# Kernel tuning notes

Measured on AMD Instinct MI355X. Metric: run time of the kernel, lower is better.

The kernel has to match this reference:

```python
import jax, jax.numpy as jnp
import numpy as np

D_MODEL = 1024
D_STATE = 16
D_CONV = 4
EXPAND = 2
D_INNER = EXPAND * D_MODEL  # 2048
B_SZ = 4
SEQ_L = 2048


def setup_inputs() -> dict:
    key = jax.random.key(0)
    ks = jax.random.split(key, 8)
    x = jax.random.normal(ks[0], (B_SZ, SEQ_L, D_MODEL), dtype=jnp.float32)
    # nn.Linear(d_model, 2*d_inner, bias=False): weight [2*d_inner, d_model]
    W_in = jax.random.normal(ks[1], (2 * D_INNER, D_MODEL), dtype=jnp.float32) * (1.0 / np.sqrt(D_MODEL))
    # depthwise Conv1d weight [d_inner, 1, d_conv] -> stored as [d_inner, d_conv]
    conv_w = jax.random.normal(ks[2], (D_INNER, D_CONV), dtype=jnp.float32) * (1.0 / np.sqrt(D_CONV))
    conv_b = jax.random.normal(ks[3], (D_INNER,), dtype=jnp.float32) * 0.01
    W_out = jax.random.normal(ks[4], (D_MODEL, D_INNER), dtype=jnp.float32) * (1.0 / np.sqrt(D_INNER))
    A = jnp.eye(D_STATE, dtype=jnp.float32)
    Bmat = jax.random.normal(ks[5], (D_STATE, D_INNER), dtype=jnp.float32) * 0.01
    Cmat = jax.random.normal(ks[6], (D_STATE, D_INNER), dtype=jnp.float32) * 0.01
    return {"x": x, "W_in": W_in, "conv_w": conv_w, "conv_b": conv_b,
            "W_out": W_out, "A": A, "Bmat": Bmat, "Cmat": Cmat}


def _causal_depthwise_conv(x_bld, conv_w, conv_b):
    # x_bld: [B, L, C]; conv_w: [C, k]; matches torch Conv1d(groups=C, padding=k-1) sliced to [:L]
    C, k = conv_w.shape
    lhs = jnp.transpose(x_bld, (0, 2, 1))            # [B, C, L]
    rhs = conv_w[:, None, :]                          # [C, 1, k]
    out = jax.lax.conv_general_dilated(
        lhs, rhs, window_strides=(1,), padding=[(k - 1, 0)],
        feature_group_count=C,
        dimension_numbers=("NCH", "OIH", "NCH"))
    out = out + conv_b[None, :, None]
    return jnp.transpose(out, (0, 2, 1))              # [B, L, C]


def reference(x, W_in, conv_w, conv_b, W_out, A, Bmat, Cmat):
    B, L, _ = x.shape
    d_state = A.shape[0]
    xz = x @ W_in.T                                   # [B, L, 2*d_inner]
    x_part, z = jnp.split(xz, 2, axis=-1)             # each [B, L, d_inner]
    x_conv = jax.nn.silu(_causal_depthwise_conv(x_part, conv_w, conv_b))
    # precompute input drive u_t = x_t @ B.T for all t
    u = jnp.einsum("bld,sd->bls", x_part, Bmat)       # [B, L, d_state]

    def step(s, u_t):                                 # s: [B, d_state]
        s = s @ A.T + u_t
        return s, s

    s0 = jnp.zeros((B, d_state), dtype=x.dtype)
    _, states = jax.lax.scan(step, s0, jnp.transpose(u, (1, 0, 2)))  # [L, B, d_state]
    states = jnp.transpose(states, (1, 0, 2))         # [B, L, d_state]
    state_proj = jnp.einsum("bls,sd->bld", states, Cmat)  # [B, L, d_inner]
    y = (x_conv + state_proj) * jax.nn.sigmoid(z)     # [B, L, d_inner]
    return y @ W_out.T                                # [B, L, d_model]
```

## Files before the change

### kernel.cpp

```cpp
#include <hip/hip_runtime.h>

#define D_MODEL 1024
#define D_STATE 16
#define D_CONV  4
#define D_INNER 2048
#define B_SZ    4
#define SEQ_L   2048
#define ROWS    (B_SZ * SEQ_L)
#define N_XZ    (2 * D_INNER)

typedef unsigned short u16;
typedef unsigned int   u32;
typedef float f32x4 __attribute__((ext_vector_type(4)));
typedef short s16x8 __attribute__((ext_vector_type(8)));
typedef u16   u16x8 __attribute__((ext_vector_type(8)));
typedef u16   u16x4 __attribute__((ext_vector_type(4)));

__device__ __forceinline__ u16 f2bf(float f) {
  union { float f; u32 u; } v; v.f = f;
  u32 r = v.u + 0x7fffu + ((v.u >> 16) & 1u);
  return (u16)(r >> 16);
}
__device__ __forceinline__ float bf2f(u16 h) {
  union { u32 u; float f; } v; v.u = ((u32)h) << 16; return v.f;
}
__device__ __forceinline__ float sigmoidf_(float x) {
  return 1.0f / (1.0f + __expf(-x));
}

__global__ __launch_bounds__(256) void k_f2bf4(
    const float* __restrict__ a, u16* __restrict__ ao, int na4,
    const float* __restrict__ b, u16* __restrict__ bo, int nb4,
    const float* __restrict__ c, u16* __restrict__ co, int nc4,
    const float* __restrict__ e, u16* __restrict__ eo, int ne4)
{
  int i = blockIdx.x * 256 + threadIdx.x;
  const float* s; u16* d; int j;
  if (i < na4)                              { s = a; d = ao; j = i; }
  else if (i - na4 < nb4)                   { s = b; d = bo; j = i - na4; }
  else if (i - na4 - nb4 < nc4)             { s = c; d = co; j = i - na4 - nb4; }
  else if (i - na4 - nb4 - nc4 < ne4)       { s = e; d = eo; j = i - na4 - nb4 - nc4; }
  else return;
  f32x4 v = ((const f32x4*)s)[j];
  u16x4 o;
  o[0] = f2bf(v[0]); o[1] = f2bf(v[1]); o[2] = f2bf(v[2]); o[3] = f2bf(v[3]);
  ((u16x4*)d)[j] = o;
}

template<bool OUT_BF16>
__global__ __launch_bounds__(256, 2) void k_gemm_f(
    const u16* __restrict__ A,
    const u16* __restrict__ B,
    void* __restrict__ Cv,
    int M, int N, int K, int nbx)
{
  __shared__ __align__(16) u16 lA[3][128 * 32];
  __shared__ __align__(16) u16 lB[3][256 * 32];

  const int t    = threadIdx.x;
  const int lane = t & 63;
  const int wave = t >> 6;
  const int wr   = wave >> 1;
  const int wc   = wave & 1;
  const int lrow = lane & 15;
  const int lch  = lane >> 4;

  const int xcd = blockIdx.x & 7;
  const int sub = blockIdx.x >> 3;
  const int msz = (M >> 7) >> 2;
  const int nsz = nbx >> 1;
  const int sm  = sub / nsz;
  const int sn  = sub - sm * nsz;
  const int bm  = ((xcd >> 1) * msz + sm) * 128;
  const int bn  = ((xcd & 1) * nsz + sn) * 256;
  const int NT  = K / 32;

  const int ca0 = t, ca1 = t + 256;
  const u16* srcA0 = A + (size_t)(bm + (ca0 >> 2)) * K + ((ca0 & 3) ^ ((ca0 >> 3) & 3)) * 8;
  const u16* srcA1 = A + (size_t)(bm + (ca1 >> 2)) * K + ((ca1 & 3) ^ ((ca1 >> 3) & 3)) * 8;
  const u16* srcB[4];
#pragma unroll
  for (int i = 0; i < 4; ++i) {
    int c = t + i * 256;
    srcB[i] = B + (size_t)(bn + (c >> 2)) * K + ((c & 3) ^ ((c >> 3) & 3)) * 8;
  }

  auto stageA = [&](int sl, int kt) {
    __builtin_amdgcn_global_load_lds(
        (const __attribute__((address_space(1))) void*)(srcA0 + kt * 32),
        (__attribute__((address_space(3))) void*)&lA[sl][ca0 * 8], 16, 0, 0);
    __builtin_amdgcn_global_load_lds(
        (const __attribute__((address_space(1))) void*)(srcA1 + kt * 32),
        (__attribute__((address_space(3))) void*)&lA[sl][ca1 * 8], 16, 0, 0);
  };
  auto stageB = [&](int sl, int kt) {
#pragma unroll
    for (int i = 0; i < 4; ++i) {
      int c = t + i * 256;
      __builtin_amdgcn_global_load_lds(
          (const __attribute__((address_space(1))) void*)(srcB[i] + kt * 32),
          (__attribute__((address_space(3))) void*)&lB[sl][c * 8], 16, 0, 0);
    }
  };

  u32 offA[4], offB[8];
#pragma unroll
  for (int m = 0; m < 4; ++m) {
    int ra = wr * 64 + m * 16 + lrow;
    offA[m] = (u32)(ra * 64 + ((lch ^ ((ra >> 1) & 3)) << 4));
  }
#pragma unroll
  for (int n = 0; n < 8; ++n) {
    int rb = wc * 128 + n * 16 + lrow;
    offB[n] = (u32)(rb * 64 + ((lch ^ ((rb >> 1) & 3)) << 4));
  }
  const u32 baseA = (u32)(size_t)(__attribute__((address_space(3))) void*)&lA[0][0];
  const u32 baseB = (u32)(size_t)(__attribute__((address_space(3))) void*)&lB[0][0];

  f32x4 acc[4][8] = {};
  s16x8 av[4], bv[8];

  stageA(0, 0); stageB(0, 0);
  stageA(1, 1); stageB(1, 1);
  asm volatile("s_waitcnt vmcnt(6)" ::: "memory");
  __builtin_amdgcn_sched_barrier(0);
  __builtin_amdgcn_s_barrier();

  int slot = 0;
  for (int tt = 0; tt < NT; ++tt) {
    const int nslot = (slot == 0) ? 2 : slot - 1;
    const u32 bA = baseA + (u32)slot * 8192u;
    const u32 bB = baseB + (u32)slot * 16384u;
    const bool st = (tt + 2 < NT);
#pragma unroll
    for (int m = 0; m < 4; ++m) {
      u32 ad = bA + offA[m];
      asm volatile("ds_read_b128 %0, %1" : "=v"(av[m]) : "v"(ad));
    }
#pragma unroll
    for (int n = 0; n < 4; ++n) {
      u32 ad = bB + offB[n];
      asm volatile("ds_read_b128 %0, %1" : "=v"(bv[n]) : "v"(ad));
    }
    if (st) stageA(nslot, tt + 2);
    __builtin_amdgcn_sched_barrier(0);
    __builtin_amdgcn_s_barrier();
    asm volatile("s_waitcnt lgkmcnt(0)" ::: "memory");
    __builtin_amdgcn_sched_barrier(0);
    __builtin_amdgcn_s_setprio(1);
#pragma unroll
    for (int m = 0; m < 4; ++m)
#pragma unroll
      for (int n = 0; n < 4; ++n)
        acc[m][n] = __builtin_amdgcn_mfma_f32_16x16x32_bf16(
            av[m], bv[n], acc[m][n], 0, 0, 0);
    __builtin_amdgcn_s_setprio(0);
    __builtin_amdgcn_sched_barrier(0);
    __builtin_amdgcn_s_barrier();
#pragma unroll
    for (int n = 4; n < 8; ++n) {
      u32 ad = bB + offB[n];
      asm volatile("ds_read_b128 %0, %1" : "=v"(bv[n]) : "v"(ad));
    }
    if (st) stageB(nslot, tt + 2);
    __builtin_amdgcn_sched_barrier(0);
    __builtin_amdgcn_s_barrier();
    asm volatile("s_waitcnt lgkmcnt(0)" ::: "memory");
    __builtin_amdgcn_sched_barrier(0);
    __builtin_amdgcn_s_setprio(1);
#pragma unroll
    for (int m = 0; m < 4; ++m)
#pragma unroll
      for (int n = 4; n < 8; ++n)
        acc[m][n] = __builtin_amdgcn_mfma_f32_16x16x32_bf16(
            av[m], bv[n], acc[m][n], 0, 0, 0);
    __builtin_amdgcn_s_setprio(0);
    if (st)                asm volatile("s_waitcnt vmcnt(6)" ::: "memory");
    else if (tt + 1 < NT)  asm volatile("s_waitcnt vmcnt(0)" ::: "memory");
    __builtin_amdgcn_sched_barrier(0);
    __builtin_amdgcn_s_barrier();
    slot = (slot == 2) ? 0 : slot + 1;
  }

  const int crow0 = (lane >> 4) * 4;
  if constexpr (OUT_BF16) {
    u16* C = (u16*)Cv;
#pragma unroll
    for (int m = 0; m < 4; ++m)
#pragma unroll
      for (int n = 0; n < 8; ++n)
#pragma unroll
        for (int r = 0; r < 4; ++r) {
          int row = bm + wr * 64 + m * 16 + crow0 + r;
          int col = bn + wc * 128 + n * 16 + lrow;
          C[(size_t)row * N + col] = f2bf(acc[m][n][r]);
        }
  } else {
    float* C = (float*)Cv;
#pragma unroll
    for (int m = 0; m < 4; ++m)
#pragma unroll
      for (int n = 0; n < 8; ++n)
#pragma unroll
        for (int r = 0; r < 4; ++r) {
          int row = bm + wr * 64 + m * 16 + crow0 + r;
          int col = bn + wc * 128 + n * 16 + lrow;
          C[(size_t)row * N + col] = acc[m][n][r];
        }
  }
}

__global__ __launch_bounds__(256) void k_u_mfma(
    const u16* __restrict__ xz,
    const u16* __restrict__ Bbf,
    float* __restrict__ u)
{
  const int lane = threadIdx.x & 63;
  const int wave = threadIdx.x >> 6;
  const int row0 = blockIdx.x * 64 + wave * 16;
  const int ar   = lane & 15;
  const int ak   = (lane >> 4) * 8;
  const u16* xp = xz + (size_t)(row0 + ar) * N_XZ + ak;
  const u16* bp = Bbf + (size_t)ar * D_INNER + ak;
  f32x4 acc = {};
#pragma unroll 8
  for (int k = 0; k < D_INNER; k += 32) {
    s16x8 av = *(const s16x8*)(xp + k);
    s16x8 bv = *(const s16x8*)(bp + k);
    acc = __builtin_amdgcn_mfma_f32_16x16x32_bf16(av, bv, acc, 0, 0, 0);
  }
#pragma unroll
  for (int r = 0; r < 4; ++r)
    u[(size_t)(row0 + (lane >> 4) * 4 + r) * D_STATE + ar] = acc[r];
}

__global__ __launch_bounds__(64) void k_scan(
    const float* __restrict__ u, float* __restrict__ states)
{
  const int blk  = blockIdx.x;
  const int b    = blk >> 4;
  const int s    = blk & 15;
  const int lane = threadIdx.x;
  const float* up = u + (size_t)b * SEQ_L * D_STATE + s;
  float* sp = states + (size_t)b * SEQ_L * D_STATE + s;
  const int t0 = lane * (SEQ_L / 64);
  float v[32];
  float run = 0.0f;
#pragma unroll
  for (int i = 0; i < 32; ++i) { run += up[(size_t)(t0 + i) * D_STATE]; v[i] = run; }
  float tot = run;
  float pre = tot;
#pragma unroll
  for (int off = 1; off < 64; off <<= 1) {
    float n = __shfl_up(pre, off);
    if (lane >= off) pre += n;
  }
  pre -= tot;
#pragma unroll
  for (int i = 0; i < 32; ++i) sp[(size_t)(t0 + i) * D_STATE] = v[i] + pre;
}

__global__ __launch_bounds__(256) void k_fused_y(
    const u16* __restrict__ xz, const float* __restrict__ conv_w,
    const float* __restrict__ conv_b, const float* __restrict__ states,
    const float* __restrict__ Cmat, u16* __restrict__ y)
{
  const int t    = threadIdx.x;
  const int row0 = blockIdx.x * 4;
  const int l0   = row0 & (SEQ_L - 1);
  const int d0   = t * 8;

  float xin[7][8];
#pragma unroll
  for (int r = 0; r < 7; ++r) {
    int l = l0 + r - 3;
    if (l >= 0) {
      u16x8 v = *(const u16x8*)(xz + (size_t)(row0 + r - 3) * N_XZ + d0);
#pragma unroll
      for (int j = 0; j < 8; ++j) xin[r][j] = bf2f(v[j]);
    } else {
#pragma unroll
      for (int j = 0; j < 8; ++j) xin[r][j] = 0.0f;
    }
  }

  float cw[8][4];
#pragma unroll
  for (int j = 0; j < 8; ++j) {
    f32x4 w = ((const f32x4*)conv_w)[d0 + j];
#pragma unroll
    for (int k = 0; k < 4; ++k) cw[j][k] = w[k];
  }
  f32x4 cb0 = *(const f32x4*)(conv_b + d0);
  f32x4 cb1 = *(const f32x4*)(conv_b + d0 + 4);

  float xc[4][8];
#pragma unroll
  for (int rr = 0; rr < 4; ++rr)
#pragma unroll
    for (int j = 0; j < 8; ++j) {
      float v = (j < 4) ? cb0[j] : cb1[j - 4];
#pragma unroll
      for (int k = 0; k < 4; ++k) v += xin[rr + k][j] * cw[j][k];
      xc[rr][j] = v * sigmoidf_(v);
    }

  float st[4][16];
#pragma unroll
  for (int rr = 0; rr < 4; ++rr) {
    const f32x4* s4 = (const f32x4*)(states + (size_t)(row0 + rr) * D_STATE);
#pragma unroll
    for (int q = 0; q < 4; ++q) {
      f32x4 v = s4[q];
      st[rr][q * 4 + 0] = v[0]; st[rr][q * 4 + 1] = v[1];
      st[rr][q * 4 + 2] = v[2]; st[rr][q * 4 + 3] = v[3];
    }
  }
  float sp[4][8] = {};
#pragma unroll
  for (int s = 0; s < 16; ++s) {
    const float* cp = Cmat + (size_t)s * D_INNER + d0;
    f32x4 c0 = *(const f32x4*)cp;
    f32x4 c1 = *(const f32x4*)(cp + 4);
#pragma unroll
    for (int rr = 0; rr < 4; ++rr)
#pragma unroll
      for (int j = 0; j < 4; ++j) {
        sp[rr][j]     += st[rr][s] * c0[j];
        sp[rr][4 + j] += st[rr][s] * c1[j];
      }
  }
#pragma unroll
  for (int rr = 0; rr < 4; ++rr) {
    u16x8 zv = *(const u16x8*)(xz + (size_t)(row0 + rr) * N_XZ + D_INNER + d0);
    u16x8 o;
#pragma unroll
    for (int j = 0; j < 8; ++j)
      o[j] = f2bf((xc[rr][j] + sp[rr][j]) * sigmoidf_(bf2f(zv[j])));
    *(u16x8*)(y + (size_t)(row0 + rr) * D_INNER + d0) = o;
  }
}

extern "C" void kernel_launch(void* const* d_in, const int* in_sizes, int n_in,
                              void* d_out, int out_size, void* d_ws, size_t ws_size,
                              hipStream_t stream) {
  const float* x      = (const float*)d_in[0];
  const float* W_in   = (const float*)d_in[1];
  const float* conv_w = (const float*)d_in[2];
  const float* conv_b = (const float*)d_in[3];
  const float* W_out  = (const float*)d_in[4];
  const float* Bmat   = (const float*)d_in[6];
  const float* Cmat   = (const float*)d_in[7];
  float* out = (float*)d_out;

  char* ws = (char*)d_ws;
  u16*   xzbf   = (u16*)  (ws + 0);
  u16*   ybf    = (u16*)  (ws + 67108864);
  u16*   xbf    = (u16*)  (ws + 100663296);
  u16*   wibf   = (u16*)  (ws + 117440512);
  u16*   wobf   = (u16*)  (ws + 125829120);
  float* u      = (float*)(ws + 130023424);
  float* states = (float*)(ws + 130547712);
  u16*   bmbf   = (u16*)  (ws + 131072000);

  {
    int na4 = ROWS * D_MODEL / 4, nb4 = N_XZ * D_MODEL / 4,
        nc4 = D_MODEL * D_INNER / 4, ne4 = D_STATE * D_INNER / 4;
    int tot = na4 + nb4 + nc4 + ne4;
    k_f2bf4<<<(tot + 255) / 256, 256, 0, stream>>>(
        x, xbf, na4, W_in, wibf, nb4, W_out, wobf, nc4, Bmat, bmbf, ne4);
  }

  k_gemm_f<true><<<1024, 256, 0, stream>>>(xbf, wibf, xzbf, ROWS, N_XZ, D_MODEL, N_XZ / 256);

  k_u_mfma<<<ROWS / 64, 256, 0, stream>>>(xzbf, bmbf, u);
  k_scan<<<B_SZ * D_STATE, 64, 0, stream>>>(u, states);

  k_fused_y<<<ROWS / 4, 256, 0, stream>>>(xzbf, conv_w, conv_b, states, Cmat, ybf);

  k_gemm_f<false><<<256, 256, 0, stream>>>(ybf, wobf, out, ROWS, D_MODEL, D_INNER, D_MODEL / 256);
}
```

Measured before the change: 191.7 us.

## Add 256x256 tile GEMM for input projection and retile u/fused-y kernels

```diff
diff --git a/kernel.cpp b/kernel.cpp
--- a/kernel.cpp
+++ b/kernel.cpp
@@ -47,12 +47,124 @@
   ((u16x4*)d)[j] = o;
 }
 
+__global__ __launch_bounds__(512, 2) void k_gbig(
+    const u16* __restrict__ A,
+    const u16* __restrict__ B,
+    u16* __restrict__ C,
+    int M, int N, int K, int nbx)
+{
+  __shared__ __align__(16) u16 lA[2][256 * 32];
+  __shared__ __align__(16) u16 lB[2][256 * 32];
+
+  const int t    = threadIdx.x;
+  const int lane = t & 63;
+  const int wave = t >> 6;
+  const int wr   = wave >> 2;
+  const int wc   = wave & 3;
+  const int lrow = lane & 15;
+  const int kch  = lane >> 4;
+
+  const int xcd = blockIdx.x & 7;
+  const int sub = blockIdx.x >> 3;
+  const int msz = (M >> 8) >> 2;
+  const int nsz = nbx >> 1;
+  const int sm  = sub / nsz;
+  const int sn  = sub - sm * nsz;
+  const int bm  = ((xcd >> 1) * msz + sm) * 256;
+  const int bn  = ((xcd & 1) * nsz + sn) * 256;
+  const int NT  = K / 32;
+
+  const int c0 = t, c1 = t + 512;
+  const int r0 = c0 >> 2, ch0 = c0 & 3;
+  const int r1 = c1 >> 2, ch1 = c1 & 3;
+  const u16* srcA0 = A + (size_t)(bm + r0) * K + ((ch0 ^ ((r0 >> 1) & 3)) << 3);
+  const u16* srcA1 = A + (size_t)(bm + r1) * K + ((ch1 ^ ((r1 >> 1) & 3)) << 3);
+  const u16* srcB0 = B + (size_t)(bn + r0) * K + ((ch0 ^ ((r0 >> 1) & 3)) << 3);
+  const u16* srcB1 = B + (size_t)(bn + r1) * K + ((ch1 ^ ((r1 >> 1) & 3)) << 3);
+
+  auto stage = [&](int buf, int kt) {
+    __builtin_amdgcn_global_load_lds(
+        (const __attribute__((address_space(1))) void*)(srcA0 + kt * 32),
+        (__attribute__((address_space(3))) void*)&lA[buf][c0 * 8], 16, 0, 0);
+    __builtin_amdgcn_global_load_lds(
+        (const __attribute__((address_space(1))) void*)(srcA1 + kt * 32),
+        (__attribute__((address_space(3))) void*)&lA[buf][c1 * 8], 16, 0, 0);
+    __builtin_amdgcn_global_load_lds(
+        (const __attribute__((address_space(1))) void*)(srcB0 + kt * 32),
+        (__attribute__((address_space(3))) void*)&lB[buf][c0 * 8], 16, 0, 0);
+    __builtin_amdgcn_global_load_lds(
+        (const __attribute__((address_space(1))) void*)(srcB1 + kt * 32),
+        (__attribute__((address_space(3))) void*)&lB[buf][c1 * 8], 16, 0, 0);
+  };
+
+  u32 aoff[8], boff[4];
+#pragma unroll
+  for (int mi = 0; mi < 8; ++mi) {
+    int row = wr * 128 + mi * 16 + lrow;
+    aoff[mi] = (u32)(row * 64 + ((kch ^ ((row >> 1) & 3)) << 4));
+  }
+#pragma unroll
+  for (int ni = 0; ni < 4; ++ni) {
+    int row = wc * 64 + ni * 16 + lrow;
+    boff[ni] = (u32)(row * 64 + ((kch ^ ((row >> 1) & 3)) << 4));
+  }
+  const u32 baseA = (u32)(size_t)(__attribute__((address_space(3))) void*)&lA[0][0];
+  const u32 baseB = (u32)(size_t)(__attribute__((address_space(3))) void*)&lB[0][0];
+
+  f32x4 acc[8][4] = {};
+  s16x8 av[8], bv[4];
+
+  stage(0, 0);
+  asm volatile("s_waitcnt vmcnt(0)" ::: "memory");
+  __builtin_amdgcn_s_barrier();
+
+  for (int tt = 0; tt < NT; ++tt) {
+    const int cur = tt & 1;
+    const u32 bA = baseA + (u32)cur * 16384u;
+    const u32 bB = baseB + (u32)cur * 16384u;
+    const bool s1 = (tt + 1 < NT);
+
+#pragma unroll
+    for (int mi = 0; mi < 8; ++mi) {
+      u32 ad = bA + aoff[mi];
+      asm volatile("ds_read_b128 %0, %1" : "=v"(av[mi]) : "v"(ad));
+    }
+#pragma unroll
+    for (int ni = 0; ni < 4; ++ni) {
+      u32 ad = bB + boff[ni];
+      asm volatile("ds_read_b128 %0, %1" : "=v"(bv[ni]) : "v"(ad));
+    }
+    if (s1) stage(cur ^ 1, tt + 1);
+    asm volatile("s_waitcnt lgkmcnt(0)" ::: "memory");
+    __builtin_amdgcn_sched_barrier(0);
+    __builtin_amdgcn_s_setprio(1);
+#pragma unroll
+    for (int mi = 0; mi < 8; ++mi)
+#pragma unroll
+      for (int ni = 0; ni < 4; ++ni)
+        acc[mi][ni] = __builtin_amdgcn_mfma_f32_16x16x32_bf16(av[mi], bv[ni], acc[mi][ni], 0, 0, 0);
+    __builtin_amdgcn_s_setprio(0);
+    if (s1) asm volatile("s_waitcnt vmcnt(0)" ::: "memory");
+    __builtin_amdgcn_s_barrier();
+  }
+
+  const int crow0 = (lane >> 4) * 4;
+#pragma unroll
+  for (int mi = 0; mi < 8; ++mi)
+#pragma unroll
+    for (int ni = 0; ni < 4; ++ni)
+#pragma unroll
+      for (int r = 0; r < 4; ++r) {
+        int row = bm + wr * 128 + mi * 16 + crow0 + r;
+        int col = bn + wc * 64 + ni * 16 + lrow;
+        C[(size_t)row * N + col] = f2bf(acc[mi][ni][r]);
+      }
+}
+
 template<bool OUT_BF16>
 __global__ __launch_bounds__(256, 2) void k_gemm_f(
-    const u16* __restrict__ A,
-    const u16* __restrict__ B,
-    void* __restrict__ Cv,
-    int M, int N, int K, int nbx)
+    const u16* __restrict__ A, const u16* __restrict__ B,
+    void* __restrict__ Cv, int M, int N, int K, int nbx)
 {
   __shared__ __align__(16) u16 lA[3][128 * 32];
   __shared__ __align__(16) u16 lB[3][256 * 32];
@@ -123,7 +235,6 @@
   stageA(0, 0); stageB(0, 0);
   stageA(1, 1); stageB(1, 1);
   asm volatile("s_waitcnt vmcnt(6)" ::: "memory");
-  __builtin_amdgcn_sched_barrier(0);
   __builtin_amdgcn_s_barrier();
 
   int slot = 0;
@@ -133,17 +244,16 @@
     const u32 bB = baseB + (u32)slot * 16384u;
     const bool st = (tt + 2 < NT);
 #pragma unroll
+    for (int n = 0; n < 4; ++n) {
+      u32 ad = bB + offB[n];
+      asm volatile("ds_read_b128 %0, %1" : "=v"(bv[n]) : "v"(ad));
+    }
+#pragma unroll
     for (int m = 0; m < 4; ++m) {
       u32 ad = bA + offA[m];
       asm volatile("ds_read_b128 %0, %1" : "=v"(av[m]) : "v"(ad));
     }
-#pragma unroll
-    for (int n = 0; n < 4; ++n) {
-      u32 ad = bB + offB[n];
-      asm volatile("ds_read_b128 %0, %1" : "=v"(bv[n]) : "v"(ad));
-    }
     if (st) stageA(nslot, tt + 2);
-    __builtin_amdgcn_sched_barrier(0);
     __builtin_amdgcn_s_barrier();
     asm volatile("s_waitcnt lgkmcnt(0)" ::: "memory");
     __builtin_amdgcn_sched_barrier(0);
@@ -152,10 +262,8 @@
     for (int m = 0; m < 4; ++m)
 #pragma unroll
       for (int n = 0; n < 4; ++n)
-        acc[m][n] = __builtin_amdgcn_mfma_f32_16x16x32_bf16(
-            av[m], bv[n], acc[m][n], 0, 0, 0);
+        acc[m][n] = __builtin_amdgcn_mfma_f32_16x16x32_bf16(av[m], bv[n], acc[m][n], 0, 0, 0);
     __builtin_amdgcn_s_setprio(0);
-    __builtin_amdgcn_sched_barrier(0);
     __builtin_amdgcn_s_barrier();
 #pragma unroll
     for (int n = 4; n < 8; ++n) {
@@ -163,7 +271,6 @@
       asm volatile("ds_read_b128 %0, %1" : "=v"(bv[n]) : "v"(ad));
     }
     if (st) stageB(nslot, tt + 2);
-    __builtin_amdgcn_sched_barrier(0);
     __builtin_amdgcn_s_barrier();
     asm volatile("s_waitcnt lgkmcnt(0)" ::: "memory");
     __builtin_amdgcn_sched_barrier(0);
@@ -172,12 +279,10 @@
     for (int m = 0; m < 4; ++m)
 #pragma unroll
       for (int n = 4; n < 8; ++n)
-        acc[m][n] = __builtin_amdgcn_mfma_f32_16x16x32_bf16(
-            av[m], bv[n], acc[m][n], 0, 0, 0);
+        acc[m][n] = __builtin_amdgcn_mfma_f32_16x16x32_bf16(av[m], bv[n], acc[m][n], 0, 0, 0);
     __builtin_amdgcn_s_setprio(0);
     if (st)                asm volatile("s_waitcnt vmcnt(6)" ::: "memory");
     else if (tt + 1 < NT)  asm volatile("s_waitcnt vmcnt(0)" ::: "memory");
-    __builtin_amdgcn_sched_barrier(0);
     __builtin_amdgcn_s_barrier();
     slot = (slot == 2) ? 0 : slot + 1;
   }
@@ -210,28 +315,29 @@
   }
 }
 
-__global__ __launch_bounds__(256) void k_u_mfma(
-    const u16* __restrict__ xz,
-    const u16* __restrict__ Bbf,
+__global__ __launch_bounds__(64) void k_u_mfma(
+    const u16* __restrict__ xz, const u16* __restrict__ Bbf,
     float* __restrict__ u)
 {
-  const int lane = threadIdx.x & 63;
-  const int wave = threadIdx.x >> 6;
-  const int row0 = blockIdx.x * 64 + wave * 16;
+  const int lane = threadIdx.x;
+  const int row0 = blockIdx.x * 16;
   const int ar   = lane & 15;
   const int ak   = (lane >> 4) * 8;
   const u16* xp = xz + (size_t)(row0 + ar) * N_XZ + ak;
   const u16* bp = Bbf + (size_t)ar * D_INNER + ak;
-  f32x4 acc = {};
-#pragma unroll 8
-  for (int k = 0; k < D_INNER; k += 32) {
-    s16x8 av = *(const s16x8*)(xp + k);
-    s16x8 bv = *(const s16x8*)(bp + k);
-    acc = __builtin_amdgcn_mfma_f32_16x16x32_bf16(av, bv, acc, 0, 0, 0);
+  f32x4 acc0 = {}, acc1 = {};
+#pragma unroll 4
+  for (int k = 0; k < D_INNER; k += 64) {
+    s16x8 a0 = *(const s16x8*)(xp + k);
+    s16x8 b0 = *(const s16x8*)(bp + k);
+    s16x8 a1 = *(const s16x8*)(xp + k + 32);
+    s16x8 b1 = *(const s16x8*)(bp + k + 32);
+    acc0 = __builtin_amdgcn_mfma_f32_16x16x32_bf16(a0, b0, acc0, 0, 0, 0);
+    acc1 = __builtin_amdgcn_mfma_f32_16x16x32_bf16(a1, b1, acc1, 0, 0, 0);
   }
 #pragma unroll
   for (int r = 0; r < 4; ++r)
-    u[(size_t)(row0 + (lane >> 4) * 4 + r) * D_STATE + ar] = acc[r];
+    u[(size_t)(row0 + (lane >> 4) * 4 + r) * D_STATE + ar] = acc0[r] + acc1[r];
 }
 
 __global__ __launch_bounds__(64) void k_scan(
@@ -265,24 +371,8 @@
     const float* __restrict__ conv_b, const float* __restrict__ states,
     const float* __restrict__ Cmat, u16* __restrict__ y)
 {
-  const int t    = threadIdx.x;
-  const int row0 = blockIdx.x * 4;
-  const int l0   = row0 & (SEQ_L - 1);
-  const int d0   = t * 8;
-
-  float xin[7][8];
-#pragma unroll
-  for (int r = 0; r < 7; ++r) {
-    int l = l0 + r - 3;
-    if (l >= 0) {
-      u16x8 v = *(const u16x8*)(xz + (size_t)(row0 + r - 3) * N_XZ + d0);
-#pragma unroll
-      for (int j = 0; j < 8; ++j) xin[r][j] = bf2f(v[j]);
-    } else {
-#pragma unroll
-      for (int j = 0; j < 8; ++j) xin[r][j] = 0.0f;
-    }
-  }
+  const int t  = threadIdx.x;
+  const int d0 = t * 8;
 
   float cw[8][4];
 #pragma unroll
@@ -294,50 +384,69 @@
   f32x4 cb0 = *(const f32x4*)(conv_b + d0);
   f32x4 cb1 = *(const f32x4*)(conv_b + d0 + 4);
 
-  float xc[4][8];
-#pragma unroll
-  for (int rr = 0; rr < 4; ++rr)
-#pragma unroll
-    for (int j = 0; j < 8; ++j) {
-      float v = (j < 4) ? cb0[j] : cb1[j - 4];
-#pragma unroll
-      for (int k = 0; k < 4; ++k) v += xin[rr + k][j] * cw[j][k];
-      xc[rr][j] = v * sigmoidf_(v);
-    }
-
-  float st[4][16];
-#pragma unroll
-  for (int rr = 0; rr < 4; ++rr) {
-    const f32x4* s4 = (const f32x4*)(states + (size_t)(row0 + rr) * D_STATE);
-#pragma unroll
-    for (int q = 0; q < 4; ++q) {
-      f32x4 v = s4[q];
-      st[rr][q * 4 + 0] = v[0]; st[rr][q * 4 + 1] = v[1];
-      st[rr][q * 4 + 2] = v[2]; st[rr][q * 4 + 3] = v[3];
-    }
-  }
-  float sp[4][8] = {};
-#pragma unroll
-  for (int s = 0; s < 16; ++s) {
-    const float* cp = Cmat + (size_t)s * D_INNER + d0;
-    f32x4 c0 = *(const f32x4*)cp;
-    f32x4 c1 = *(const f32x4*)(cp + 4);
+  for (int ch = 0; ch < 4; ++ch) {
+    const int row0 = blockIdx.x * 16 + ch * 4;
+    const int l0   = row0 & (SEQ_L - 1);
+
+    float xin[7][8];
+#pragma unroll
+    for (int r = 0; r < 7; ++r) {
+      int l = l0 + r - 3;
+      if (l >= 0) {
+        u16x8 v = *(const u16x8*)(xz + (size_t)(row0 + r - 3) * N_XZ + d0);
+#pragma unroll
+        for (int j = 0; j < 8; ++j) xin[r][j] = bf2f(v[j]);
+      } else {
+#pragma unroll
+        for (int j = 0; j < 8; ++j) xin[r][j] = 0.0f;
+      }
+    }
+
+    float xc[4][8];
 #pragma unroll
     for (int rr = 0; rr < 4; ++rr)
 #pragma unroll
-      for (int j = 0; j < 4; ++j) {
-        sp[rr][j]     += st[rr][s] * c0[j];
-        sp[rr][4 + j] += st[rr][s] * c1[j];
+      for (int j = 0; j < 8; ++j) {
+        float v = (j < 4) ? cb0[j] : cb1[j - 4];
+#pragma unroll
+        for (int k = 0; k < 4; ++k) v += xin[rr + k][j] * cw[j][k];
+        xc[rr][j] = v * sigmoidf_(v);
       }
-  }
-#pragma unroll
-  for (int rr = 0; rr < 4; ++rr) {
-    u16x8 zv = *(const u16x8*)(xz + (size_t)(row0 + rr) * N_XZ + D_INNER + d0);
-    u16x8 o;
-#pragma unroll
-    for (int j = 0; j < 8; ++j)
-      o[j] = f2bf((xc[rr][j] + sp[rr][j]) * sigmoidf_(bf2f(zv[j])));
-    *(u16x8*)(y + (size_t)(row0 + rr) * D_INNER + d0) = o;
+
+    float st[4][16];
+#pragma unroll
+    for (int rr = 0; rr < 4; ++rr) {
+      const f32x4* s4 = (const f32x4*)(states + (size_t)(row0 + rr) * D_STATE);
+#pragma unroll
+      for (int q = 0; q < 4; ++q) {
+        f32x4 v = s4[q];
+        st[rr][q * 4 + 0] = v[0]; st[rr][q * 4 + 1] = v[1];
+        st[rr][q * 4 + 2] = v[2]; st[rr][q * 4 + 3] = v[3];
+      }
+    }
+    float sp[4][8] = {};
+#pragma unroll
+    for (int s = 0; s < 16; ++s) {
+      const float* cp = Cmat + (size_t)s * D_INNER + d0;
+      f32x4 c0 = *(const f32x4*)cp;
+      f32x4 c1 = *(const f32x4*)(cp + 4);
+#pragma unroll
+      for (int rr = 0; rr < 4; ++rr)
+#pragma unroll
+        for (int j = 0; j < 4; ++j) {
+          sp[rr][j]     += st[rr][s] * c0[j];
+          sp[rr][4 + j] += st[rr][s] * c1[j];
+        }
+    }
+#pragma unroll
+    for (int rr = 0; rr < 4; ++rr) {
+      u16x8 zv = *(const u16x8*)(xz + (size_t)(row0 + rr) * N_XZ + D_INNER + d0);
+      u16x8 o;
+#pragma unroll
+      for (int j = 0; j < 8; ++j)
+        o[j] = f2bf((xc[rr][j] + sp[rr][j]) * sigmoidf_(bf2f(zv[j])));
+      *(u16x8*)(y + (size_t)(row0 + rr) * D_INNER + d0) = o;
+    }
   }
 }
 
@@ -371,12 +480,12 @@
         x, xbf, na4, W_in, wibf, nb4, W_out, wobf, nc4, Bmat, bmbf, ne4);
   }
 
-  k_gemm_f<true><<<1024, 256, 0, stream>>>(xbf, wibf, xzbf, ROWS, N_XZ, D_MODEL, N_XZ / 256);
-
-  k_u_mfma<<<ROWS / 64, 256, 0, stream>>>(xzbf, bmbf, u);
+  k_gbig<<<512, 512, 0, stream>>>(xbf, wibf, xzbf, ROWS, N_XZ, D_MODEL, N_XZ / 256);
+
+  k_u_mfma<<<ROWS / 16, 64, 0, stream>>>(xzbf, bmbf, u);
   k_scan<<<B_SZ * D_STATE, 64, 0, stream>>>(u, states);
 
-  k_fused_y<<<ROWS / 4, 256, 0, stream>>>(xzbf, conv_w, conv_b, states, Cmat, ybf);
+  k_fused_y<<<ROWS / 16, 256, 0, stream>>>(xzbf, conv_w, conv_b, states, Cmat, ybf);
 
   k_gemm_f<false><<<256, 256, 0, stream>>>(ybf, wobf, out, ROWS, D_MODEL, D_INNER, D_MODEL / 256);
 }
```

New measurement: 183.3 us. 4.4% less time.
